# Kernel optimization log

Measured on AMD Instinct MI355X. Metric: run time of the kernel, lower is better.

## Reference

```python
import jax, jax.numpy as jnp
import numpy as np

BINS = 10
LOSS_WEIGHT = 1.0
B = 8388608  # batch size
C = 2        # class num (hardcoded in the torch module's one-hot scatter)


def setup_inputs() -> dict:
    key = jax.random.key(0)
    k1, k2, k3 = jax.random.split(key, 3)
    pred = jax.random.normal(k1, (B, C), dtype=jnp.float32)
    target = jax.random.randint(k2, (B,), 0, 2, dtype=jnp.int64)
    # label_weight: 1 if valid, 0 if ignored (random 0/1 mask as float)
    label_weight = jax.random.randint(k3, (B, C), 0, 2).astype(jnp.float32)
    return {"pred": pred, "target": target, "label_weight": label_weight}


def reference(pred, target, label_weight):
    # one-hot target: torch scatter_(1, target, 1) over 2 classes
    t = jax.nn.one_hot(target, C, dtype=jnp.float32)  # [B, 2]
    # gradient norm g = |softmax(pred).detach() - target_onehot|
    g = jnp.abs(jax.lax.stop_gradient(jax.nn.softmax(pred, axis=1)) - t)  # [B, 2]
    valid = label_weight > 0
    valid_f = valid.astype(jnp.float32)
    total = jnp.maximum(valid_f.sum(), 1.0)
    # bin index: edges are i/bins with last edge nudged by 1e-6; uniform bins so
    # floor(g*bins) clipped to bins-1 reproduces the loop's (>= low) & (<= high)
    # assignment (ties on interior edges resolve to the upper bin, matching the
    # later-iteration overwrite in the torch loop).
    bin_ids = jnp.minimum((g * BINS).astype(jnp.int32), BINS - 1)  # [B, 2]
    # per-bin valid counts (histogram)
    counts = jnp.zeros((BINS,), jnp.float32).at[bin_ids].add(valid_f)
    n = jnp.maximum((counts > 0).sum().astype(jnp.float32), 1.0)
    # GHM weights: total / num_in_bin / n for valid entries, 0 otherwise
    w = jnp.where(valid, total / jnp.maximum(counts[bin_ids], 1.0) / n, 0.0)
    w = jax.lax.stop_gradient(w)
    # weighted BCE-with-logits, reduction='sum'
    bce = jnp.maximum(pred, 0.0) - pred * t + jnp.log1p(jnp.exp(-jnp.abs(pred)))
    loss = (w * bce).sum() / total
    return loss * LOSS_WEIGHT
```

## Files before the change

### kernel.cpp

```cpp
#include <hip/hip_runtime.h>

#define BINS 10
#define TPB  256
#define NCOPY 8


__device__ __forceinline__ void ghm_row(float p0, float p1, int t, float w0, float w1,
                                        unsigned long long* hrow)
{
    float z = (t == 0) ? (p1 - p0) : (p0 - p1);
    float e = __expf(-z);
    float g = __fdividef(1.0f, 1.0f + e);
    int bin = min((int)(g * 10.0f), BINS - 1);

    float l0 = __logf(1.0f + __expf(-fabsf(p0)));
    float l1 = __logf(1.0f + __expf(-fabsf(p1)));
    float bce0 = fmaxf(p0, 0.0f) - ((t == 0) ? p0 : 0.0f) + l0;
    float bce1 = fmaxf(p1, 0.0f) - ((t == 1) ? p1 : 0.0f) + l1;

    bool v0 = (w0 > 0.0f);
    bool v1 = (w1 > 0.0f);
    float wsum = (v0 ? bce0 : 0.0f) + (v1 ? bce1 : 0.0f);
    unsigned long long cnt = (unsigned long long)((int)v0 + (int)v1);
    unsigned long long packed = (cnt << 48)
        | (unsigned long long)(unsigned int)(wsum * 1048576.0f + 0.5f);
    if (packed) atomicAdd(&hrow[bin], packed);
}

__global__ __launch_bounds__(TPB) void ghm_stage1(
    const float* __restrict__ pred, const int* __restrict__ target,
    const float* __restrict__ lw, unsigned long long* __restrict__ partial, int B)
{
    __shared__ unsigned long long h[NCOPY][BINS];
    if (threadIdx.x < NCOPY * BINS)
        ((unsigned long long*)h)[threadIdx.x] = 0ULL;
    __syncthreads();

    unsigned long long* hrow = h[threadIdx.x >> 5];

    const float4* p4 = (const float4*)pred;
    const float4* w4 = (const float4*)lw;
    const int2*   t2 = (const int2*)target;

    const int npairs = B >> 1;
    const int stride = gridDim.x * blockDim.x;
    for (int i = blockIdx.x * blockDim.x + threadIdx.x; i < npairs; i += stride) {
        float4 p = p4[i];
        float4 w = w4[i];
        int2   t = t2[i];
        ghm_row(p.x, p.y, t.x, w.x, w.y, hrow);
        ghm_row(p.z, p.w, t.y, w.z, w.w, hrow);
    }
    if ((B & 1) && blockIdx.x == 0 && threadIdx.x == 0) {
        int r = B - 1;
        ghm_row(pred[2 * r], pred[2 * r + 1], target[r], lw[2 * r], lw[2 * r + 1], h[0]);
    }
    __syncthreads();

    if (threadIdx.x < BINS) {
        unsigned long long v = 0;
#pragma unroll
        for (int c = 0; c < NCOPY; ++c) v += h[c][threadIdx.x];
        partial[blockIdx.x * BINS + threadIdx.x] = v;
    }
}

__global__ __launch_bounds__(TPB) void ghm_stage2(
    const unsigned long long* __restrict__ partial, float* __restrict__ out, int nb)
{
    double dsum[BINS];
    double dcnt[BINS];
#pragma unroll
    for (int b = 0; b < BINS; ++b) { dsum[b] = 0.0; dcnt[b] = 0.0; }

    for (int i = threadIdx.x; i < nb; i += TPB) {
#pragma unroll
        for (int b = 0; b < BINS; ++b) {
            unsigned long long p = partial[i * BINS + b];
            dcnt[b] += (double)(p >> 48);
            dsum[b] += (double)(p & ((1ULL << 48) - 1)) * (1.0 / 1048576.0);
        }
    }

#pragma unroll
    for (int b = 0; b < BINS; ++b) {
        for (int off = 32; off > 0; off >>= 1) {
            dsum[b] += __shfl_down(dsum[b], off);
            dcnt[b] += __shfl_down(dcnt[b], off);
        }
    }

    __shared__ double ss[4][BINS];
    __shared__ double sc[4][BINS];
    const int wid  = threadIdx.x >> 6;
    const int lane = threadIdx.x & 63;
    if (lane == 0) {
#pragma unroll
        for (int b = 0; b < BINS; ++b) { ss[wid][b] = dsum[b]; sc[wid][b] = dcnt[b]; }
    }
    __syncthreads();

    if (threadIdx.x == 0) {
        double loss = 0.0;
        int n = 0;
        for (int b = 0; b < BINS; ++b) {
            double S = ss[0][b] + ss[1][b] + ss[2][b] + ss[3][b];
            double C = sc[0][b] + sc[1][b] + sc[2][b] + sc[3][b];
            if (C > 0.0) { ++n; loss += S / C; }
        }
        if (n == 0) n = 1;
        out[0] = (float)(loss / (double)n);
    }
}

extern "C" void kernel_launch(void* const* d_in, const int* in_sizes, int n_in,
                              void* d_out, int out_size, void* d_ws, size_t ws_size,
                              hipStream_t stream)
{
    const float* pred   = (const float*)d_in[0];
    const int*   target = (const int*)d_in[1];
    const float* lw     = (const float*)d_in[2];
    const int B = in_sizes[1];

    int nb = 2048;
    size_t need = (size_t)nb * BINS * sizeof(unsigned long long);
    if (ws_size < need) nb = (int)(ws_size / (BINS * sizeof(unsigned long long)));

    unsigned long long* partial = (unsigned long long*)d_ws;

    ghm_stage1<<<nb, TPB, 0, stream>>>(pred, target, lw, partial, B);
    ghm_stage2<<<1, TPB, 0, stream>>>(partial, (float*)d_out, nb);
}
```

Baseline: 40.53 us.

## Simplify GHM math, merge same-bin atomics, unroll loads, widen histogram copies

Rewrites the per-row math so g comes from a product of two exponentials and the masked BCE sum becomes a single log of a product, cutting transcendental calls per row. When both rows handled by a thread land in the same bin, their packed values are combined into one shared atomic. The grid-stride loop is unrolled by four with all loads issued first to raise memory-level parallelism, and the shared histogram is replicated 16 ways instead of 8 to reduce atomic contention. The log-of-product form may lose precision or overflow for large logits.

```diff
diff --git a/kernel.cpp b/kernel.cpp
--- a/kernel.cpp
+++ b/kernel.cpp
@@ -2,29 +2,43 @@
 
 #define BINS 10
 #define TPB  256
-#define NCOPY 8
+#define NBLK 2048
+#define NCOPY 16
 
-
-__device__ __forceinline__ void ghm_row(float p0, float p1, int t, float w0, float w1,
-                                        unsigned long long* hrow)
+__device__ __forceinline__ unsigned long long ghm_pack(float p0, float p1, int t,
+                                                       float w0, float w1, int* bin)
 {
-    float z = (t == 0) ? (p1 - p0) : (p0 - p1);
-    float e = __expf(-z);
-    float g = __fdividef(1.0f, 1.0f + e);
-    int bin = min((int)(g * 10.0f), BINS - 1);
-
-    float l0 = __logf(1.0f + __expf(-fabsf(p0)));
-    float l1 = __logf(1.0f + __expf(-fabsf(p1)));
-    float bce0 = fmaxf(p0, 0.0f) - ((t == 0) ? p0 : 0.0f) + l0;
-    float bce1 = fmaxf(p1, 0.0f) - ((t == 1) ? p1 : 0.0f) + l1;
+    bool tz = (t == 0);
+    float x0 = tz ? -p0 : p0;
+    float x1 = tz ?  p1 : -p1;
+    float e0 = __expf(x0);
+    float e1 = __expf(x1);
+    float m  = e0 * e1;
+    float g  = __fdividef(m, 1.0f + m);
+    *bin = min((int)(g * 10.0f), BINS - 1);
 
     bool v0 = (w0 > 0.0f);
     bool v1 = (w1 > 0.0f);
-    float wsum = (v0 ? bce0 : 0.0f) + (v1 ? bce1 : 0.0f);
+    float a = v0 ? (1.0f + e0) : 1.0f;
+    float b = v1 ? (1.0f + e1) : 1.0f;
+    float wsum = __logf(a * b);
     unsigned long long cnt = (unsigned long long)((int)v0 + (int)v1);
-    unsigned long long packed = (cnt << 48)
-        | (unsigned long long)(unsigned int)(wsum * 1048576.0f + 0.5f);
-    if (packed) atomicAdd(&hrow[bin], packed);
+    return (cnt << 48) | (unsigned long long)(unsigned int)(wsum * 1048576.0f + 0.5f);
+}
+
+__device__ __forceinline__ void ghm_2rows(float4 p, int2 t, float4 w,
+                                          unsigned long long* hrow)
+{
+    int b0, b1;
+    unsigned long long c0 = ghm_pack(p.x, p.y, t.x, w.x, w.y, &b0);
+    unsigned long long c1 = ghm_pack(p.z, p.w, t.y, w.z, w.w, &b1);
+    if (b0 == b1) {
+        unsigned long long cs = c0 + c1;
+        if (cs) atomicAdd(&hrow[b0], cs);
+    } else {
+        if (c0) atomicAdd(&hrow[b0], c0);
+        if (c1) atomicAdd(&hrow[b1], c1);
+    }
 }
 
 __global__ __launch_bounds__(TPB) void ghm_stage1(
@@ -32,28 +46,46 @@
     const float* __restrict__ lw, unsigned long long* __restrict__ partial, int B)
 {
     __shared__ unsigned long long h[NCOPY][BINS];
-    if (threadIdx.x < NCOPY * BINS)
-        ((unsigned long long*)h)[threadIdx.x] = 0ULL;
+    for (int k = threadIdx.x; k < NCOPY * BINS; k += TPB)
+        ((unsigned long long*)h)[k] = 0ULL;
     __syncthreads();
 
-    unsigned long long* hrow = h[threadIdx.x >> 5];
+    unsigned long long* hrow = h[threadIdx.x >> 4];
 
     const float4* p4 = (const float4*)pred;
     const float4* w4 = (const float4*)lw;
     const int2*   t2 = (const int2*)target;
+    const int npairs = B >> 1;
+    const int stride = (int)gridDim.x * TPB;
+    int i = blockIdx.x * TPB + threadIdx.x;
 
-    const int npairs = B >> 1;
-    const int stride = gridDim.x * blockDim.x;
-    for (int i = blockIdx.x * blockDim.x + threadIdx.x; i < npairs; i += stride) {
-        float4 p = p4[i];
-        float4 w = w4[i];
-        int2   t = t2[i];
-        ghm_row(p.x, p.y, t.x, w.x, w.y, hrow);
-        ghm_row(p.z, p.w, t.y, w.z, w.w, hrow);
+    for (; i + 3 * stride < npairs; i += 4 * stride) {
+        float4 pa = p4[i];
+        float4 pb = p4[i + stride];
+        float4 pc = p4[i + 2 * stride];
+        float4 pd = p4[i + 3 * stride];
+        float4 wa = w4[i];
+        float4 wb = w4[i + stride];
+        float4 wc = w4[i + 2 * stride];
+        float4 wd = w4[i + 3 * stride];
+        int2   ta = t2[i];
+        int2   tb = t2[i + stride];
+        int2   tc = t2[i + 2 * stride];
+        int2   td = t2[i + 3 * stride];
+        ghm_2rows(pa, ta, wa, hrow);
+        ghm_2rows(pb, tb, wb, hrow);
+        ghm_2rows(pc, tc, wc, hrow);
+        ghm_2rows(pd, td, wd, hrow);
     }
+    for (; i < npairs; i += stride)
+        ghm_2rows(p4[i], t2[i], w4[i], hrow);
+
     if ((B & 1) && blockIdx.x == 0 && threadIdx.x == 0) {
         int r = B - 1;
-        ghm_row(pred[2 * r], pred[2 * r + 1], target[r], lw[2 * r], lw[2 * r + 1], h[0]);
+        int bb;
+        unsigned long long cc = ghm_pack(pred[2 * r], pred[2 * r + 1], target[r],
+                                         lw[2 * r], lw[2 * r + 1], &bb);
+        if (cc) atomicAdd(&h[0][bb], cc);
     }
     __syncthreads();
 
@@ -68,8 +100,7 @@
 __global__ __launch_bounds__(TPB) void ghm_stage2(
     const unsigned long long* __restrict__ partial, float* __restrict__ out, int nb)
 {
-    double dsum[BINS];
-    double dcnt[BINS];
+    double dsum[BINS], dcnt[BINS];
 #pragma unroll
     for (int b = 0; b < BINS; ++b) { dsum[b] = 0.0; dcnt[b] = 0.0; }
 
@@ -122,7 +153,7 @@
     const float* lw     = (const float*)d_in[2];
     const int B = in_sizes[1];
 
-    int nb = 2048;
+    int nb = NBLK;
     size_t need = (size_t)nb * BINS * sizeof(unsigned long long);
     if (ws_size < need) nb = (int)(ws_size / (BINS * sizeof(unsigned long long)));
 
```

After: 41.06 us, median of 2. About the same (+1.3%).
